# Optimization experiments

Measured on AMD Instinct MI355X. Metric: run time of the kernel, lower is better.

Reference implementation:

```python
import jax, jax.numpy as jnp
import numpy as np

N_TOKENS = 2048
D_MODEL = 1024
D_FF = 4 * D_MODEL
N_EXPERTS = 8
TOP_K = 2


def setup_inputs() -> dict:
    key = jax.random.key(0)
    k_x, k_g, k_w1, k_w2 = jax.random.split(key, 4)
    x = jax.random.normal(k_x, (N_TOKENS, D_MODEL), dtype=jnp.float32)
    # torch Linear stores weight as [out_features, in_features]
    gate_w = jax.random.normal(k_g, (N_EXPERTS, D_MODEL), dtype=jnp.float32) * 0.02
    w1 = jax.random.normal(k_w1, (N_EXPERTS, D_FF, D_MODEL), dtype=jnp.float32) * 0.02
    w2 = jax.random.normal(k_w2, (N_EXPERTS, D_MODEL, D_FF), dtype=jnp.float32) * 0.02
    return {"x": x, "gate_w": gate_w, "w1": w1, "w2": w2}


def reference(x, gate_w, w1, w2):
    # Gating: top-2 logits, softmax over just the selected two logits
    logits = jnp.einsum("nd,ed->ne", x, gate_w)            # [N, E]
    top_vals, top_idx = jax.lax.top_k(logits, TOP_K)         # [N, 2]
    top_w = jax.nn.softmax(top_vals, axis=-1)                # [N, 2]

    # Combine weight per (token, expert): sum of gate weights where routed
    cw = jnp.sum(jax.nn.one_hot(top_idx, N_EXPERTS, dtype=x.dtype)
                 * top_w[..., None], axis=1)                 # [N, E]

    # Per-expert FFN, masked-combined (single-process path of the module)
    out = jnp.zeros_like(x)
    for e in range(N_EXPERTS):
        h = jax.nn.gelu(x @ w1[e].T, approximate=False)      # [N, 4d] (nn.GELU = exact erf)
        y = h @ w2[e].T                                      # [N, d]
        out = out + cw[:, e:e + 1] * y
    return out
```

## Files before the change

kernel.cpp:

```cpp
#include <hip/hip_runtime.h>
#include <hip/hip_bf16.h>

typedef short short8 __attribute__((ext_vector_type(8)));
typedef float f32x4 __attribute__((ext_vector_type(4)));

#define N_TOKENS 2048
#define D_MODEL 1024
#define D_FF 4096
#define N_EXPERTS 8
#define TOTAL_SLOTS (N_TOKENS * 2)
#define BK 32
#define SPLITK2 4
#define KC2 (D_FF / SPLITK2)

static __device__ __forceinline__ unsigned int f2u(float f) {
    union { float f; unsigned int u; } v; v.f = f; return v.u;
}

static __device__ __forceinline__ unsigned short f2bf(float f) {
    unsigned int u = f2u(f);
    unsigned int r = (u + 0x7fffu + ((u >> 16) & 1u)) >> 16;
    return (unsigned short)r;
}

static __device__ __forceinline__ unsigned int pk2bf(float a, float b) {
    __hip_bfloat162 t = __float22bfloat162_rn(float2{a, b});
    unsigned int u;
    __builtin_memcpy(&u, &t, 4);
    return u;
}

typedef __attribute__((address_space(1))) const unsigned int GU;
typedef __attribute__((address_space(3))) unsigned int LU;
static __device__ __forceinline__ void gload_lds16(const void* g, void* l) {
    __builtin_amdgcn_global_load_lds((GU*)g, (LU*)l, 16, 0, 0);
}

__global__ __launch_bounds__(256) void cvt_x_kernel(const float* __restrict__ x,
                                                    unsigned short* __restrict__ xb) {
    int i = (blockIdx.x * 256 + threadIdx.x) * 4;
    if (i >= N_TOKENS * D_MODEL) return;
    float4 f = *(const float4*)(x + i);
    uint2 o;
    o.x = pk2bf(f.x, f.y);
    o.y = pk2bf(f.z, f.w);
    *(uint2*)(xb + i) = o;
}

__global__ __launch_bounds__(64) void gate_kernel(const float* __restrict__ x,
                                                  const float* __restrict__ gw,
                                                  int* __restrict__ counts,
                                                  int* __restrict__ tok_e,
                                                  float* __restrict__ tok_w) {
    const int n = blockIdx.x;
    const int lane = threadIdx.x;
    float p[N_EXPERTS];
#pragma unroll
    for (int e = 0; e < N_EXPERTS; ++e) p[e] = 0.f;
    const float* xr = x + n * D_MODEL;
    for (int d = lane; d < D_MODEL; d += 64) {
        float xv = xr[d];
#pragma unroll
        for (int e = 0; e < N_EXPERTS; ++e) p[e] += xv * gw[e * D_MODEL + d];
    }
#pragma unroll
    for (int e = 0; e < N_EXPERTS; ++e) {
        float v = p[e];
        for (int o = 32; o > 0; o >>= 1) v += __shfl_down(v, o);
        p[e] = v;
    }
    if (lane == 0) {
        int b1 = 0; float v1 = p[0];
        for (int e = 1; e < N_EXPERTS; ++e) if (p[e] > v1) { v1 = p[e]; b1 = e; }
        int b2 = -1; float v2 = -1e30f;
        for (int e = 0; e < N_EXPERTS; ++e) if (e != b1 && p[e] > v2) { v2 = p[e]; b2 = e; }
        float e2 = __expf(v2 - v1);
        float s = 1.f + e2;
        tok_e[n * 2 + 0] = b1; tok_w[n * 2 + 0] = 1.f / s;
        tok_e[n * 2 + 1] = b2; tok_w[n * 2 + 1] = e2 / s;
        atomicAdd(&counts[b1], 1);
        atomicAdd(&counts[b2], 1);
    }
}

__global__ void scan_kernel(const int* __restrict__ counts,
                            int* __restrict__ offsets, int* __restrict__ fill) {
    if (threadIdx.x == 0 && blockIdx.x == 0) {
        int s = 0;
        for (int e = 0; e < N_EXPERTS; ++e) { offsets[e] = s; fill[e] = s; s += counts[e]; }
    }
}

__global__ __launch_bounds__(256) void route_kernel(const int* __restrict__ tok_e,
                                                    const float* __restrict__ tok_w,
                                                    int* __restrict__ fill,
                                                    int* __restrict__ rows_tok,
                                                    float* __restrict__ rows_w) {
    int i = blockIdx.x * 256 + threadIdx.x;
    if (i >= TOTAL_SLOTS) return;
    int e = tok_e[i];
    float w = tok_w[i];
    int pos = atomicAdd(&fill[e], 1);
    rows_tok[pos] = i >> 1;
    rows_w[pos] = w;
}

__global__ __launch_bounds__(256, 3) void gemm1_kernel(const unsigned short* __restrict__ xb,
                                                       const float* __restrict__ w1,
                                                       const int* __restrict__ counts,
                                                       const int* __restrict__ offsets,
                                                       const int* __restrict__ rows_tok,
                                                       unsigned short* __restrict__ h) {
    const int e = blockIdx.z;
    const int cnt = counts[e];
    const int mt = blockIdx.y;
    if (mt * 128 >= cnt) return;
    const int off = offsets[e];
    const int nt = blockIdx.x;

    __shared__ unsigned short As[2][128 * 32];
    __shared__ unsigned short Bs[2][128 * 32];

    const int tid = threadIdx.x;
    const int lane = tid & 63;
    const int wave = tid >> 6;
    const int wm = wave >> 1, wn = wave & 1;

    const int arow = wave * 32 + (lane >> 2);
    const int ac8 = lane & 3;
    int r0 = off + mt * 128 + arow;
    int r1 = r0 + 16;
    r0 = min(r0, TOTAL_SLOTS - 1);
    r1 = min(r1, TOTAL_SLOTS - 1);
    const unsigned short* ag0 = xb + (size_t)rows_tok[r0] * D_MODEL + ac8 * 8;
    const unsigned short* ag1 = xb + (size_t)rows_tok[r1] * D_MODEL + ac8 * 8;
    unsigned short* al0_0 = &As[0][(wave * 32) * 32];
    unsigned short* al1_0 = &As[0][(wave * 32 + 16) * 32];
    unsigned short* al0_1 = &As[1][(wave * 32) * 32];
    unsigned short* al1_1 = &As[1][(wave * 32 + 16) * 32];

    const int brow = tid >> 1, bcol = (tid & 1) * 16;
    const float* bg = w1 + (size_t)e * (D_FF * D_MODEL) + (size_t)(nt * 128 + brow) * D_MODEL + bcol;

    f32x4 acc[4][4];
#pragma unroll
    for (int i = 0; i < 4; ++i)
#pragma unroll
        for (int j = 0; j < 4; ++j) acc[i][j] = (f32x4){0.f, 0.f, 0.f, 0.f};

    {
        gload_lds16(ag0, al0_0);
        gload_lds16(ag1, al1_0);
        float4 fb0 = *(const float4*)(bg + 0);
        float4 fb1 = *(const float4*)(bg + 4);
        float4 fb2 = *(const float4*)(bg + 8);
        float4 fb3 = *(const float4*)(bg + 12);
        unsigned int bp[8];
        bp[0] = pk2bf(fb0.x, fb0.y); bp[1] = pk2bf(fb0.z, fb0.w);
        bp[2] = pk2bf(fb1.x, fb1.y); bp[3] = pk2bf(fb1.z, fb1.w);
        bp[4] = pk2bf(fb2.x, fb2.y); bp[5] = pk2bf(fb2.z, fb2.w);
        bp[6] = pk2bf(fb3.x, fb3.y); bp[7] = pk2bf(fb3.z, fb3.w);
        *(uint4*)&Bs[0][brow * 32 + bcol]     = *(uint4*)&bp[0];
        *(uint4*)&Bs[0][brow * 32 + bcol + 8] = *(uint4*)&bp[4];
    }
    __syncthreads();

    const int KSTEPS = D_MODEL / BK;
#pragma unroll 2
    for (int t = 0; t < KSTEPS; ++t) {
        const int cur = t & 1;
        const bool more = (t + 1 < KSTEPS);
        float4 fb0, fb1, fb2, fb3;
        if (more) {
            const int k1 = (t + 1) * BK;
            fb0 = *(const float4*)(bg + k1 + 0);
            fb1 = *(const float4*)(bg + k1 + 4);
            fb2 = *(const float4*)(bg + k1 + 8);
            fb3 = *(const float4*)(bg + k1 + 12);
            gload_lds16(ag0 + k1, cur ? al0_0 : al0_1);
            gload_lds16(ag1 + k1, cur ? al1_0 : al1_1);
        }
        short8 af[4], bfr[4];
#pragma unroll
        for (int mi = 0; mi < 4; ++mi)
            af[mi] = *(const short8*)&As[cur][(wm * 64 + mi * 16 + (lane & 15)) * 32 + (lane >> 4) * 8];
#pragma unroll
        for (int nj = 0; nj < 4; ++nj)
            bfr[nj] = *(const short8*)&Bs[cur][(wn * 64 + nj * 16 + (lane & 15)) * 32 + (lane >> 4) * 8];
#pragma unroll
        for (int mi = 0; mi < 4; ++mi)
#pragma unroll
            for (int nj = 0; nj < 4; ++nj)
                acc[mi][nj] = __builtin_amdgcn_mfma_f32_16x16x32_bf16(af[mi], bfr[nj], acc[mi][nj], 0, 0, 0);
        if (more) {
            unsigned int bp[8];
            bp[0] = pk2bf(fb0.x, fb0.y); bp[1] = pk2bf(fb0.z, fb0.w);
            bp[2] = pk2bf(fb1.x, fb1.y); bp[3] = pk2bf(fb1.z, fb1.w);
            bp[4] = pk2bf(fb2.x, fb2.y); bp[5] = pk2bf(fb2.z, fb2.w);
            bp[6] = pk2bf(fb3.x, fb3.y); bp[7] = pk2bf(fb3.z, fb3.w);
            const int nb = cur ^ 1;
            *(uint4*)&Bs[nb][brow * 32 + bcol]     = *(uint4*)&bp[0];
            *(uint4*)&Bs[nb][brow * 32 + bcol + 8] = *(uint4*)&bp[4];
        }
        __syncthreads();
    }

    const int lr = (lane >> 4) * 4, lc = lane & 15;
#pragma unroll
    for (int mi = 0; mi < 4; ++mi) {
        const int mbase = mt * 128 + wm * 64 + mi * 16 + lr;
#pragma unroll
        for (int j = 0; j < 4; ++j) {
            const int m = mbase + j;
            if (m < cnt) {
#pragma unroll
                for (int nj = 0; nj < 4; ++nj) {
                    const int n = nt * 128 + wn * 64 + nj * 16 + lc;
                    float v = acc[mi][nj][j];
                    v = 0.5f * v * (1.0f + erff(v * 0.70710678118654752f));
                    h[(size_t)(off + m) * D_FF + n] = f2bf(v);
                }
            }
        }
    }
}

__global__ __launch_bounds__(256, 3) void gemm2_kernel(const unsigned short* __restrict__ h,
                                                       const float* __restrict__ w2,
                                                       const int* __restrict__ counts,
                                                       const int* __restrict__ offsets,
                                                       const int* __restrict__ rows_tok,
                                                       const float* __restrict__ rows_w,
                                                       float* __restrict__ out) {
    const int e = blockIdx.z >> 2;
    const int kc = blockIdx.z & 3;
    const int cnt = counts[e];
    const int mt = blockIdx.y;
    if (mt * 128 >= cnt) return;
    const int off = offsets[e];
    const int nt = blockIdx.x;

    __shared__ unsigned short As[2][128 * 32];
    __shared__ unsigned short Bs[2][128 * 32];

    const int tid = threadIdx.x;
    const int lane = tid & 63;
    const int wave = tid >> 6;
    const int wm = wave >> 1, wn = wave & 1;

    const int arow = wave * 32 + (lane >> 2);
    const int ac8 = lane & 3;
    int r0 = off + mt * 128 + arow;
    int r1 = r0 + 16;
    r0 = min(r0, TOTAL_SLOTS - 1);
    r1 = min(r1, TOTAL_SLOTS - 1);
    const unsigned short* ag0 = h + (size_t)r0 * D_FF + kc * KC2 + ac8 * 8;
    const unsigned short* ag1 = h + (size_t)r1 * D_FF + kc * KC2 + ac8 * 8;
    unsigned short* al0_0 = &As[0][(wave * 32) * 32];
    unsigned short* al1_0 = &As[0][(wave * 32 + 16) * 32];
    unsigned short* al0_1 = &As[1][(wave * 32) * 32];
    unsigned short* al1_1 = &As[1][(wave * 32 + 16) * 32];

    const int brow = tid >> 1, bcol = (tid & 1) * 16;
    const float* bg = w2 + (size_t)e * (D_MODEL * D_FF) + (size_t)(nt * 128 + brow) * D_FF
                      + kc * KC2 + bcol;

    f32x4 acc[4][4];
#pragma unroll
    for (int i = 0; i < 4; ++i)
#pragma unroll
        for (int j = 0; j < 4; ++j) acc[i][j] = (f32x4){0.f, 0.f, 0.f, 0.f};

    {
        gload_lds16(ag0, al0_0);
        gload_lds16(ag1, al1_0);
        float4 fb0 = *(const float4*)(bg + 0);
        float4 fb1 = *(const float4*)(bg + 4);
        float4 fb2 = *(const float4*)(bg + 8);
        float4 fb3 = *(const float4*)(bg + 12);
        unsigned int bp[8];
        bp[0] = pk2bf(fb0.x, fb0.y); bp[1] = pk2bf(fb0.z, fb0.w);
        bp[2] = pk2bf(fb1.x, fb1.y); bp[3] = pk2bf(fb1.z, fb1.w);
        bp[4] = pk2bf(fb2.x, fb2.y); bp[5] = pk2bf(fb2.z, fb2.w);
        bp[6] = pk2bf(fb3.x, fb3.y); bp[7] = pk2bf(fb3.z, fb3.w);
        *(uint4*)&Bs[0][brow * 32 + bcol]     = *(uint4*)&bp[0];
        *(uint4*)&Bs[0][brow * 32 + bcol + 8] = *(uint4*)&bp[4];
    }
    __syncthreads();

    const int KSTEPS = KC2 / BK;
#pragma unroll 2
    for (int t = 0; t < KSTEPS; ++t) {
        const int cur = t & 1;
        const bool more = (t + 1 < KSTEPS);
        float4 fb0, fb1, fb2, fb3;
        if (more) {
            const int k1 = (t + 1) * BK;
            fb0 = *(const float4*)(bg + k1 + 0);
            fb1 = *(const float4*)(bg + k1 + 4);
            fb2 = *(const float4*)(bg + k1 + 8);
            fb3 = *(const float4*)(bg + k1 + 12);
            gload_lds16(ag0 + k1, cur ? al0_0 : al0_1);
            gload_lds16(ag1 + k1, cur ? al1_0 : al1_1);
        }
        short8 af[4], bfr[4];
#pragma unroll
        for (int mi = 0; mi < 4; ++mi)
            af[mi] = *(const short8*)&As[cur][(wm * 64 + mi * 16 + (lane & 15)) * 32 + (lane >> 4) * 8];
#pragma unroll
        for (int nj = 0; nj < 4; ++nj)
            bfr[nj] = *(const short8*)&Bs[cur][(wn * 64 + nj * 16 + (lane & 15)) * 32 + (lane >> 4) * 8];
#pragma unroll
        for (int mi = 0; mi < 4; ++mi)
#pragma unroll
            for (int nj = 0; nj < 4; ++nj)
                acc[mi][nj] = __builtin_amdgcn_mfma_f32_16x16x32_bf16(af[mi], bfr[nj], acc[mi][nj], 0, 0, 0);
        if (more) {
            unsigned int bp[8];
            bp[0] = pk2bf(fb0.x, fb0.y); bp[1] = pk2bf(fb0.z, fb0.w);
            bp[2] = pk2bf(fb1.x, fb1.y); bp[3] = pk2bf(fb1.z, fb1.w);
            bp[4] = pk2bf(fb2.x, fb2.y); bp[5] = pk2bf(fb2.z, fb2.w);
            bp[6] = pk2bf(fb3.x, fb3.y); bp[7] = pk2bf(fb3.z, fb3.w);
            const int nb = cur ^ 1;
            *(uint4*)&Bs[nb][brow * 32 + bcol]     = *(uint4*)&bp[0];
            *(uint4*)&Bs[nb][brow * 32 + bcol + 8] = *(uint4*)&bp[4];
        }
        __syncthreads();
    }

    const int lr = (lane >> 4) * 4, lc = lane & 15;
#pragma unroll
    for (int mi = 0; mi < 4; ++mi) {
        const int mbase = mt * 128 + wm * 64 + mi * 16 + lr;
#pragma unroll
        for (int j = 0; j < 4; ++j) {
            const int m = mbase + j;
            if (m < cnt) {
                const int tok = rows_tok[off + m];
                const float w = rows_w[off + m];
#pragma unroll
                for (int nj = 0; nj < 4; ++nj) {
                    const int n = nt * 128 + wn * 64 + nj * 16 + lc;
                    atomicAdd(&out[(size_t)tok * D_MODEL + n], w * acc[mi][nj][j]);
                }
            }
        }
    }
}


extern "C" void kernel_launch(void* const* d_in, const int* in_sizes, int n_in,
                              void* d_out, int out_size, void* d_ws, size_t ws_size,
                              hipStream_t stream) {
    const float* x  = (const float*)d_in[0];
    const float* gw = (const float*)d_in[1];
    const float* w1 = (const float*)d_in[2];
    const float* w2 = (const float*)d_in[3];
    float* out = (float*)d_out;

    char* ws = (char*)d_ws;
    int*   counts   = (int*)(ws + 0);
    int*   fill     = (int*)(ws + 256);
    int*   offsets  = (int*)(ws + 512);
    int*   tok_e    = (int*)(ws + 768);
    float* tok_w    = (float*)(ws + 17152);
    int*   rows_tok = (int*)(ws + 33536);
    float* rows_w   = (float*)(ws + 49920);
    unsigned short* xb = (unsigned short*)(ws + 66560);
    unsigned short* h  = (unsigned short*)(ws + 66560 + (size_t)N_TOKENS * D_MODEL * 2);

    hipMemsetAsync(counts, 0, 32, stream);
    hipMemsetAsync(d_out, 0, (size_t)out_size * sizeof(float), stream);

    cvt_x_kernel<<<dim3((N_TOKENS * D_MODEL / 4 + 255) / 256), dim3(256), 0, stream>>>(x, xb);
    gate_kernel<<<dim3(N_TOKENS), dim3(64), 0, stream>>>(x, gw, counts, tok_e, tok_w);
    scan_kernel<<<dim3(1), dim3(64), 0, stream>>>(counts, offsets, fill);
    route_kernel<<<dim3((TOTAL_SLOTS + 255) / 256), dim3(256), 0, stream>>>(tok_e, tok_w, fill, rows_tok, rows_w);
    gemm1_kernel<<<dim3(D_FF / 128, 16, N_EXPERTS), dim3(256), 0, stream>>>(xb, w1, counts, offsets, rows_tok, h);
    gemm2_kernel<<<dim3(D_MODEL / 128, 16, N_EXPERTS * SPLITK2), dim3(256), 0, stream>>>(h, w2, counts, offsets, rows_tok, rows_w, out);
}
```

Baseline: 334.8 us.

## Deepen B-operand prefetch to two steps with manual waitcnt and barriers

Both GEMM kernels now prefetch the fp32 weight tile two K-steps ahead into ping-pong register sets, while the A tile is still loaded one step ahead directly into LDS. __syncthreads is replaced by explicit s_waitcnt lgkmcnt/vmcnt counts, s_barrier and sched_barrier so global weight loads stay in flight across the barrier. This targets the weight-load latency that was exposed each iteration. In exchange it raises register pressure and depends on hand-counted vmcnt values being correct.

```diff
diff --git a/kernel.cpp b/kernel.cpp
--- a/kernel.cpp
+++ b/kernel.cpp
@@ -105,6 +105,76 @@
     rows_w[pos] = w;
 }
 
+#define GEMM_BODY(T, CUR, BU, BF, ALn0, ALn1)                                       \
+  {                                                                                 \
+    const int t_ = (T);                                                             \
+    const bool hasA_ = (t_ + 1 < KSTEPS);                                           \
+    const bool hasB_ = (t_ + 2 < KSTEPS);                                           \
+    if (hasA_) {                                                                    \
+      const int k1_ = (t_ + 1) * BK;                                                \
+      gload_lds16(ag0 + k1_, ALn0);                                                 \
+      gload_lds16(ag1 + k1_, ALn1);                                                 \
+    }                                                                               \
+    asm volatile("" ::: "memory");                                                  \
+    if (hasB_) {                                                                    \
+      const int k2_ = (t_ + 2) * BK;                                                \
+      BU##_0 = *(const float4*)(bg + k2_ + 0);                                      \
+      BU##_1 = *(const float4*)(bg + k2_ + 4);                                      \
+      BU##_2 = *(const float4*)(bg + k2_ + 8);                                      \
+      BU##_3 = *(const float4*)(bg + k2_ + 12);                                     \
+    }                                                                               \
+    __builtin_amdgcn_sched_barrier(0);                                              \
+    short8 af_[4], bf_[4];                                                          \
+    _Pragma("unroll") for (int mi = 0; mi < 4; ++mi)                                \
+      af_[mi] = *(const short8*)&As[CUR][(wm * 64 + mi * 16 + (lane & 15)) * 32 + (lane >> 4) * 8]; \
+    _Pragma("unroll") for (int nj = 0; nj < 4; ++nj)                                \
+      bf_[nj] = *(const short8*)&Bs[CUR][(wn * 64 + nj * 16 + (lane & 15)) * 32 + (lane >> 4) * 8]; \
+    _Pragma("unroll") for (int mi = 0; mi < 4; ++mi)                                \
+      _Pragma("unroll") for (int nj = 0; nj < 4; ++nj)                              \
+        acc[mi][nj] = __builtin_amdgcn_mfma_f32_16x16x32_bf16(af_[mi], bf_[nj], acc[mi][nj], 0, 0, 0); \
+    if (hasA_) {                                                                    \
+      unsigned int bp_[8];                                                          \
+      bp_[0] = pk2bf(BF##_0.x, BF##_0.y); bp_[1] = pk2bf(BF##_0.z, BF##_0.w);       \
+      bp_[2] = pk2bf(BF##_1.x, BF##_1.y); bp_[3] = pk2bf(BF##_1.z, BF##_1.w);       \
+      bp_[4] = pk2bf(BF##_2.x, BF##_2.y); bp_[5] = pk2bf(BF##_2.z, BF##_2.w);       \
+      bp_[6] = pk2bf(BF##_3.x, BF##_3.y); bp_[7] = pk2bf(BF##_3.z, BF##_3.w);       \
+      *(uint4*)&Bs[(CUR) ^ 1][brow * 32 + bcol]     = *(uint4*)&bp_[0];             \
+      *(uint4*)&Bs[(CUR) ^ 1][brow * 32 + bcol + 8] = *(uint4*)&bp_[4];             \
+      asm volatile("s_waitcnt lgkmcnt(0)" ::: "memory");                            \
+      if (hasB_) asm volatile("s_waitcnt vmcnt(4)" ::: "memory");                   \
+      else       asm volatile("s_waitcnt vmcnt(0)" ::: "memory");                   \
+      __builtin_amdgcn_s_barrier();                                                 \
+      asm volatile("" ::: "memory");                                                \
+    }                                                                               \
+  }
+
+#define GEMM_PROLOGUE(BE)                                                           \
+  {                                                                                 \
+    gload_lds16(ag0, al0_0);                                                        \
+    gload_lds16(ag1, al1_0);                                                        \
+    asm volatile("" ::: "memory");                                                  \
+    float4 p0 = *(const float4*)(bg + 0);                                           \
+    float4 p1 = *(const float4*)(bg + 4);                                           \
+    float4 p2 = *(const float4*)(bg + 8);                                           \
+    float4 p3 = *(const float4*)(bg + 12);                                          \
+    BE##_0 = *(const float4*)(bg + BK + 0);                                         \
+    BE##_1 = *(const float4*)(bg + BK + 4);                                         \
+    BE##_2 = *(const float4*)(bg + BK + 8);                                         \
+    BE##_3 = *(const float4*)(bg + BK + 12);                                        \
+    __builtin_amdgcn_sched_barrier(0);                                              \
+    unsigned int bp_[8];                                                            \
+    bp_[0] = pk2bf(p0.x, p0.y); bp_[1] = pk2bf(p0.z, p0.w);                         \
+    bp_[2] = pk2bf(p1.x, p1.y); bp_[3] = pk2bf(p1.z, p1.w);                         \
+    bp_[4] = pk2bf(p2.x, p2.y); bp_[5] = pk2bf(p2.z, p2.w);                         \
+    bp_[6] = pk2bf(p3.x, p3.y); bp_[7] = pk2bf(p3.z, p3.w);                         \
+    *(uint4*)&Bs[0][brow * 32 + bcol]     = *(uint4*)&bp_[0];                       \
+    *(uint4*)&Bs[0][brow * 32 + bcol + 8] = *(uint4*)&bp_[4];                       \
+    asm volatile("s_waitcnt lgkmcnt(0)" ::: "memory");                              \
+    asm volatile("s_waitcnt vmcnt(4)" ::: "memory");                                \
+    __builtin_amdgcn_s_barrier();                                                   \
+    asm volatile("" ::: "memory");                                                  \
+  }
+
 __global__ __launch_bounds__(256, 3) void gemm1_kernel(const unsigned short* __restrict__ xb,
                                                        const float* __restrict__ w1,
                                                        const int* __restrict__ counts,
@@ -148,61 +218,14 @@
 #pragma unroll
         for (int j = 0; j < 4; ++j) acc[i][j] = (f32x4){0.f, 0.f, 0.f, 0.f};
 
-    {
-        gload_lds16(ag0, al0_0);
-        gload_lds16(ag1, al1_0);
-        float4 fb0 = *(const float4*)(bg + 0);
-        float4 fb1 = *(const float4*)(bg + 4);
-        float4 fb2 = *(const float4*)(bg + 8);
-        float4 fb3 = *(const float4*)(bg + 12);
-        unsigned int bp[8];
-        bp[0] = pk2bf(fb0.x, fb0.y); bp[1] = pk2bf(fb0.z, fb0.w);
-        bp[2] = pk2bf(fb1.x, fb1.y); bp[3] = pk2bf(fb1.z, fb1.w);
-        bp[4] = pk2bf(fb2.x, fb2.y); bp[5] = pk2bf(fb2.z, fb2.w);
-        bp[6] = pk2bf(fb3.x, fb3.y); bp[7] = pk2bf(fb3.z, fb3.w);
-        *(uint4*)&Bs[0][brow * 32 + bcol]     = *(uint4*)&bp[0];
-        *(uint4*)&Bs[0][brow * 32 + bcol + 8] = *(uint4*)&bp[4];
-    }
-    __syncthreads();
+    float4 bEn_0{0,0,0,0}, bEn_1{0,0,0,0}, bEn_2{0,0,0,0}, bEn_3{0,0,0,0};
+    float4 bOn_0{0,0,0,0}, bOn_1{0,0,0,0}, bOn_2{0,0,0,0}, bOn_3{0,0,0,0};
 
     const int KSTEPS = D_MODEL / BK;
-#pragma unroll 2
-    for (int t = 0; t < KSTEPS; ++t) {
-        const int cur = t & 1;
-        const bool more = (t + 1 < KSTEPS);
-        float4 fb0, fb1, fb2, fb3;
-        if (more) {
-            const int k1 = (t + 1) * BK;
-            fb0 = *(const float4*)(bg + k1 + 0);
-            fb1 = *(const float4*)(bg + k1 + 4);
-            fb2 = *(const float4*)(bg + k1 + 8);
-            fb3 = *(const float4*)(bg + k1 + 12);
-            gload_lds16(ag0 + k1, cur ? al0_0 : al0_1);
-            gload_lds16(ag1 + k1, cur ? al1_0 : al1_1);
-        }
-        short8 af[4], bfr[4];
-#pragma unroll
-        for (int mi = 0; mi < 4; ++mi)
-            af[mi] = *(const short8*)&As[cur][(wm * 64 + mi * 16 + (lane & 15)) * 32 + (lane >> 4) * 8];
-#pragma unroll
-        for (int nj = 0; nj < 4; ++nj)
-            bfr[nj] = *(const short8*)&Bs[cur][(wn * 64 + nj * 16 + (lane & 15)) * 32 + (lane >> 4) * 8];
-#pragma unroll
-        for (int mi = 0; mi < 4; ++mi)
-#pragma unroll
-            for (int nj = 0; nj < 4; ++nj)
-                acc[mi][nj] = __builtin_amdgcn_mfma_f32_16x16x32_bf16(af[mi], bfr[nj], acc[mi][nj], 0, 0, 0);
-        if (more) {
-            unsigned int bp[8];
-            bp[0] = pk2bf(fb0.x, fb0.y); bp[1] = pk2bf(fb0.z, fb0.w);
-            bp[2] = pk2bf(fb1.x, fb1.y); bp[3] = pk2bf(fb1.z, fb1.w);
-            bp[4] = pk2bf(fb2.x, fb2.y); bp[5] = pk2bf(fb2.z, fb2.w);
-            bp[6] = pk2bf(fb3.x, fb3.y); bp[7] = pk2bf(fb3.z, fb3.w);
-            const int nb = cur ^ 1;
-            *(uint4*)&Bs[nb][brow * 32 + bcol]     = *(uint4*)&bp[0];
-            *(uint4*)&Bs[nb][brow * 32 + bcol + 8] = *(uint4*)&bp[4];
-        }
-        __syncthreads();
+    GEMM_PROLOGUE(bEn)
+    for (int tt = 0; tt < KSTEPS; tt += 2) {
+        GEMM_BODY(tt,     0, bOn, bEn, al0_1, al1_1)
+        GEMM_BODY(tt + 1, 1, bEn, bOn, al0_0, al1_0)
     }
 
     const int lr = (lane >> 4) * 4, lc = lane & 15;
@@ -271,61 +294,14 @@
 #pragma unroll
         for (int j = 0; j < 4; ++j) acc[i][j] = (f32x4){0.f, 0.f, 0.f, 0.f};
 
-    {
-        gload_lds16(ag0, al0_0);
-        gload_lds16(ag1, al1_0);
-        float4 fb0 = *(const float4*)(bg + 0);
-        float4 fb1 = *(const float4*)(bg + 4);
-        float4 fb2 = *(const float4*)(bg + 8);
-        float4 fb3 = *(const float4*)(bg + 12);
-        unsigned int bp[8];
-        bp[0] = pk2bf(fb0.x, fb0.y); bp[1] = pk2bf(fb0.z, fb0.w);
-        bp[2] = pk2bf(fb1.x, fb1.y); bp[3] = pk2bf(fb1.z, fb1.w);
-        bp[4] = pk2bf(fb2.x, fb2.y); bp[5] = pk2bf(fb2.z, fb2.w);
-        bp[6] = pk2bf(fb3.x, fb3.y); bp[7] = pk2bf(fb3.z, fb3.w);
-        *(uint4*)&Bs[0][brow * 32 + bcol]     = *(uint4*)&bp[0];
-        *(uint4*)&Bs[0][brow * 32 + bcol + 8] = *(uint4*)&bp[4];
-    }
-    __syncthreads();
+    float4 bEn_0{0,0,0,0}, bEn_1{0,0,0,0}, bEn_2{0,0,0,0}, bEn_3{0,0,0,0};
+    float4 bOn_0{0,0,0,0}, bOn_1{0,0,0,0}, bOn_2{0,0,0,0}, bOn_3{0,0,0,0};
 
     const int KSTEPS = KC2 / BK;
-#pragma unroll 2
-    for (int t = 0; t < KSTEPS; ++t) {
-        const int cur = t & 1;
-        const bool more = (t + 1 < KSTEPS);
-        float4 fb0, fb1, fb2, fb3;
-        if (more) {
-            const int k1 = (t + 1) * BK;
-            fb0 = *(const float4*)(bg + k1 + 0);
-            fb1 = *(const float4*)(bg + k1 + 4);
-            fb2 = *(const float4*)(bg + k1 + 8);
-            fb3 = *(const float4*)(bg + k1 + 12);
-            gload_lds16(ag0 + k1, cur ? al0_0 : al0_1);
-            gload_lds16(ag1 + k1, cur ? al1_0 : al1_1);
-        }
-        short8 af[4], bfr[4];
-#pragma unroll
-        for (int mi = 0; mi < 4; ++mi)
-            af[mi] = *(const short8*)&As[cur][(wm * 64 + mi * 16 + (lane & 15)) * 32 + (lane >> 4) * 8];
-#pragma unroll
-        for (int nj = 0; nj < 4; ++nj)
-            bfr[nj] = *(const short8*)&Bs[cur][(wn * 64 + nj * 16 + (lane & 15)) * 32 + (lane >> 4) * 8];
-#pragma unroll
-        for (int mi = 0; mi < 4; ++mi)
-#pragma unroll
-            for (int nj = 0; nj < 4; ++nj)
-                acc[mi][nj] = __builtin_amdgcn_mfma_f32_16x16x32_bf16(af[mi], bfr[nj], acc[mi][nj], 0, 0, 0);
-        if (more) {
-            unsigned int bp[8];
-            bp[0] = pk2bf(fb0.x, fb0.y); bp[1] = pk2bf(fb0.z, fb0.w);
-            bp[2] = pk2bf(fb1.x, fb1.y); bp[3] = pk2bf(fb1.z, fb1.w);
-            bp[4] = pk2bf(fb2.x, fb2.y); bp[5] = pk2bf(fb2.z, fb2.w);
-            bp[6] = pk2bf(fb3.x, fb3.y); bp[7] = pk2bf(fb3.z, fb3.w);
-            const int nb = cur ^ 1;
-            *(uint4*)&Bs[nb][brow * 32 + bcol]     = *(uint4*)&bp[0];
-            *(uint4*)&Bs[nb][brow * 32 + bcol + 8] = *(uint4*)&bp[4];
-        }
-        __syncthreads();
+    GEMM_PROLOGUE(bEn)
+    for (int tt = 0; tt < KSTEPS; tt += 2) {
+        GEMM_BODY(tt,     0, bOn, bEn, al0_1, al1_1)
+        GEMM_BODY(tt + 1, 1, bEn, bOn, al0_0, al1_0)
     }
 
     const int lr = (lane >> 4) * 4, lc = lane & 15;
```

Measured after the change: 325.0 us. 1.03x faster.

## Pre-convert expert weights to bf16 and stream them into LDS directly

Applied to the files above, without the earlier changes.

Adds a grid-stride kernel that converts w1 and w2 from fp32 to bf16 into the workspace on every call. The GEMM kernels are templated so that, when the workspace is large enough, B tiles are loaded with global_load_lds exactly like A tiles. This removes the in-loop fp32 loads, the bf16 packing and the register-staged LDS writes. It costs an extra full pass over the weights (read fp32, write bf16) before the GEMMs, and it raises the launch-bounds occupancy hint from 3 to 4.

```diff
diff --git a/kernel.cpp b/kernel.cpp
--- a/kernel.cpp
+++ b/kernel.cpp
@@ -34,6 +34,22 @@
 typedef __attribute__((address_space(3))) unsigned int LU;
 static __device__ __forceinline__ void gload_lds16(const void* g, void* l) {
     __builtin_amdgcn_global_load_lds((GU*)g, (LU*)l, 16, 0, 0);
+}
+
+__global__ __launch_bounds__(256) void cvt_w_kernel(const float* __restrict__ src,
+                                                    unsigned short* __restrict__ dst,
+                                                    int n8) {
+    int i = blockIdx.x * 256 + threadIdx.x;
+    const int stride = gridDim.x * 256;
+    for (; i < n8; i += stride) {
+        const size_t b = (size_t)i * 8;
+        float4 f0 = *(const float4*)(src + b);
+        float4 f1 = *(const float4*)(src + b + 4);
+        uint4 o;
+        o.x = pk2bf(f0.x, f0.y); o.y = pk2bf(f0.z, f0.w);
+        o.z = pk2bf(f1.x, f1.y); o.w = pk2bf(f1.z, f1.w);
+        *(uint4*)(dst + b) = o;
+    }
 }
 
 __global__ __launch_bounds__(256) void cvt_x_kernel(const float* __restrict__ x,
@@ -105,12 +121,14 @@
     rows_w[pos] = w;
 }
 
-__global__ __launch_bounds__(256, 3) void gemm1_kernel(const unsigned short* __restrict__ xb,
-                                                       const float* __restrict__ w1,
-                                                       const int* __restrict__ counts,
-                                                       const int* __restrict__ offsets,
-                                                       const int* __restrict__ rows_tok,
-                                                       unsigned short* __restrict__ h) {
+template <bool PRE>
+__global__ __launch_bounds__(256, 4) void gemm1_kernel(
+    const unsigned short* __restrict__ xb,
+    const unsigned short* __restrict__ w1b,
+    const float* __restrict__ w1f,
+    const int* __restrict__ counts, const int* __restrict__ offsets,
+    const int* __restrict__ rows_tok,
+    unsigned short* __restrict__ h) {
     const int e = blockIdx.z;
     const int cnt = counts[e];
     const int mt = blockIdx.y;
@@ -121,26 +139,21 @@
     __shared__ unsigned short As[2][128 * 32];
     __shared__ unsigned short Bs[2][128 * 32];
 
-    const int tid = threadIdx.x;
-    const int lane = tid & 63;
-    const int wave = tid >> 6;
+    const int tid = threadIdx.x, lane = tid & 63, wave = tid >> 6;
     const int wm = wave >> 1, wn = wave & 1;
 
-    const int arow = wave * 32 + (lane >> 2);
     const int ac8 = lane & 3;
-    int r0 = off + mt * 128 + arow;
+    int r0 = off + mt * 128 + wave * 32 + (lane >> 2);
     int r1 = r0 + 16;
     r0 = min(r0, TOTAL_SLOTS - 1);
     r1 = min(r1, TOTAL_SLOTS - 1);
     const unsigned short* ag0 = xb + (size_t)rows_tok[r0] * D_MODEL + ac8 * 8;
     const unsigned short* ag1 = xb + (size_t)rows_tok[r1] * D_MODEL + ac8 * 8;
-    unsigned short* al0_0 = &As[0][(wave * 32) * 32];
-    unsigned short* al1_0 = &As[0][(wave * 32 + 16) * 32];
-    unsigned short* al0_1 = &As[1][(wave * 32) * 32];
-    unsigned short* al1_1 = &As[1][(wave * 32 + 16) * 32];
-
+
+    const int bgrow = nt * 128 + wave * 32 + (lane >> 2);
+    const unsigned short* bg0 = w1b + (size_t)e * (D_FF * D_MODEL) + (size_t)bgrow * D_MODEL + ac8 * 8;
     const int brow = tid >> 1, bcol = (tid & 1) * 16;
-    const float* bg = w1 + (size_t)e * (D_FF * D_MODEL) + (size_t)(nt * 128 + brow) * D_MODEL + bcol;
+    const float* bgf = w1f + (size_t)e * (D_FF * D_MODEL) + (size_t)(nt * 128 + brow) * D_MODEL + bcol;
 
     f32x4 acc[4][4];
 #pragma unroll
@@ -148,37 +161,56 @@
 #pragma unroll
         for (int j = 0; j < 4; ++j) acc[i][j] = (f32x4){0.f, 0.f, 0.f, 0.f};
 
-    {
-        gload_lds16(ag0, al0_0);
-        gload_lds16(ag1, al1_0);
-        float4 fb0 = *(const float4*)(bg + 0);
-        float4 fb1 = *(const float4*)(bg + 4);
-        float4 fb2 = *(const float4*)(bg + 8);
-        float4 fb3 = *(const float4*)(bg + 12);
+    auto stageA = [&](int buf, int t) {
+        const int k = t * BK;
+        gload_lds16(ag0 + k, &As[buf][(wave * 32) * 32]);
+        gload_lds16(ag1 + k, &As[buf][(wave * 32 + 16) * 32]);
+    };
+    auto stageBpre = [&](int buf, int t) {
+        const int k = t * BK;
+        gload_lds16(bg0 + k, &Bs[buf][(wave * 32) * 32]);
+        gload_lds16(bg0 + 16 * D_MODEL + k, &Bs[buf][(wave * 32 + 16) * 32]);
+    };
+    auto writeBf32 = [&](int buf, const float4& f0, const float4& f1,
+                         const float4& f2, const float4& f3) {
         unsigned int bp[8];
-        bp[0] = pk2bf(fb0.x, fb0.y); bp[1] = pk2bf(fb0.z, fb0.w);
-        bp[2] = pk2bf(fb1.x, fb1.y); bp[3] = pk2bf(fb1.z, fb1.w);
-        bp[4] = pk2bf(fb2.x, fb2.y); bp[5] = pk2bf(fb2.z, fb2.w);
-        bp[6] = pk2bf(fb3.x, fb3.y); bp[7] = pk2bf(fb3.z, fb3.w);
-        *(uint4*)&Bs[0][brow * 32 + bcol]     = *(uint4*)&bp[0];
-        *(uint4*)&Bs[0][brow * 32 + bcol + 8] = *(uint4*)&bp[4];
+        bp[0] = pk2bf(f0.x, f0.y); bp[1] = pk2bf(f0.z, f0.w);
+        bp[2] = pk2bf(f1.x, f1.y); bp[3] = pk2bf(f1.z, f1.w);
+        bp[4] = pk2bf(f2.x, f2.y); bp[5] = pk2bf(f2.z, f2.w);
+        bp[6] = pk2bf(f3.x, f3.y); bp[7] = pk2bf(f3.z, f3.w);
+        *(uint4*)&Bs[buf][brow * 32 + bcol]     = *(uint4*)&bp[0];
+        *(uint4*)&Bs[buf][brow * 32 + bcol + 8] = *(uint4*)&bp[4];
+    };
+
+    stageA(0, 0);
+    if constexpr (PRE) {
+        stageBpre(0, 0);
+    } else {
+        float4 f0 = *(const float4*)(bgf + 0);
+        float4 f1 = *(const float4*)(bgf + 4);
+        float4 f2 = *(const float4*)(bgf + 8);
+        float4 f3 = *(const float4*)(bgf + 12);
+        writeBf32(0, f0, f1, f2, f3);
     }
     __syncthreads();
 
     const int KSTEPS = D_MODEL / BK;
 #pragma unroll 2
     for (int t = 0; t < KSTEPS; ++t) {
-        const int cur = t & 1;
+        const int cur = t & 1, nxt = cur ^ 1;
         const bool more = (t + 1 < KSTEPS);
-        float4 fb0, fb1, fb2, fb3;
+        float4 f0, f1, f2, f3;
         if (more) {
-            const int k1 = (t + 1) * BK;
-            fb0 = *(const float4*)(bg + k1 + 0);
-            fb1 = *(const float4*)(bg + k1 + 4);
-            fb2 = *(const float4*)(bg + k1 + 8);
-            fb3 = *(const float4*)(bg + k1 + 12);
-            gload_lds16(ag0 + k1, cur ? al0_0 : al0_1);
-            gload_lds16(ag1 + k1, cur ? al1_0 : al1_1);
+            stageA(nxt, t + 1);
+            if constexpr (PRE) {
+                stageBpre(nxt, t + 1);
+            } else {
+                const int k = (t + 1) * BK;
+                f0 = *(const float4*)(bgf + k + 0);
+                f1 = *(const float4*)(bgf + k + 4);
+                f2 = *(const float4*)(bgf + k + 8);
+                f3 = *(const float4*)(bgf + k + 12);
+            }
         }
         short8 af[4], bfr[4];
 #pragma unroll
@@ -192,15 +224,8 @@
 #pragma unroll
             for (int nj = 0; nj < 4; ++nj)
                 acc[mi][nj] = __builtin_amdgcn_mfma_f32_16x16x32_bf16(af[mi], bfr[nj], acc[mi][nj], 0, 0, 0);
-        if (more) {
-            unsigned int bp[8];
-            bp[0] = pk2bf(fb0.x, fb0.y); bp[1] = pk2bf(fb0.z, fb0.w);
-            bp[2] = pk2bf(fb1.x, fb1.y); bp[3] = pk2bf(fb1.z, fb1.w);
-            bp[4] = pk2bf(fb2.x, fb2.y); bp[5] = pk2bf(fb2.z, fb2.w);
-            bp[6] = pk2bf(fb3.x, fb3.y); bp[7] = pk2bf(fb3.z, fb3.w);
-            const int nb = cur ^ 1;
-            *(uint4*)&Bs[nb][brow * 32 + bcol]     = *(uint4*)&bp[0];
-            *(uint4*)&Bs[nb][brow * 32 + bcol + 8] = *(uint4*)&bp[4];
+        if constexpr (!PRE) {
+            if (more) writeBf32(nxt, f0, f1, f2, f3);
         }
         __syncthreads();
     }
@@ -225,13 +250,14 @@
     }
 }
 
-__global__ __launch_bounds__(256, 3) void gemm2_kernel(const unsigned short* __restrict__ h,
-                                                       const float* __restrict__ w2,
-                                                       const int* __restrict__ counts,
-                                                       const int* __restrict__ offsets,
-                                                       const int* __restrict__ rows_tok,
-                                                       const float* __restrict__ rows_w,
-                                                       float* __restrict__ out) {
+template <bool PRE>
+__global__ __launch_bounds__(256, 4) void gemm2_kernel(
+    const unsigned short* __restrict__ h,
+    const unsigned short* __restrict__ w2b,
+    const float* __restrict__ w2f,
+    const int* __restrict__ counts, const int* __restrict__ offsets,
+    const int* __restrict__ rows_tok, const float* __restrict__ rows_w,
+    float* __restrict__ out) {
     const int e = blockIdx.z >> 2;
     const int kc = blockIdx.z & 3;
     const int cnt = counts[e];
@@ -243,27 +269,21 @@
     __shared__ unsigned short As[2][128 * 32];
     __shared__ unsigned short Bs[2][128 * 32];
 
-    const int tid = threadIdx.x;
-    const int lane = tid & 63;
-    const int wave = tid >> 6;
+    const int tid = threadIdx.x, lane = tid & 63, wave = tid >> 6;
     const int wm = wave >> 1, wn = wave & 1;
 
-    const int arow = wave * 32 + (lane >> 2);
     const int ac8 = lane & 3;
-    int r0 = off + mt * 128 + arow;
+    int r0 = off + mt * 128 + wave * 32 + (lane >> 2);
     int r1 = r0 + 16;
     r0 = min(r0, TOTAL_SLOTS - 1);
     r1 = min(r1, TOTAL_SLOTS - 1);
     const unsigned short* ag0 = h + (size_t)r0 * D_FF + kc * KC2 + ac8 * 8;
     const unsigned short* ag1 = h + (size_t)r1 * D_FF + kc * KC2 + ac8 * 8;
-    unsigned short* al0_0 = &As[0][(wave * 32) * 32];
-    unsigned short* al1_0 = &As[0][(wave * 32 + 16) * 32];
-    unsigned short* al0_1 = &As[1][(wave * 32) * 32];
-    unsigned short* al1_1 = &As[1][(wave * 32 + 16) * 32];
-
+
+    const int bgrow = nt * 128 + wave * 32 + (lane >> 2);
+    const unsigned short* bg0 = w2b + (size_t)e * (D_MODEL * D_FF) + (size_t)bgrow * D_FF + kc * KC2 + ac8 * 8;
     const int brow = tid >> 1, bcol = (tid & 1) * 16;
-    const float* bg = w2 + (size_t)e * (D_MODEL * D_FF) + (size_t)(nt * 128 + brow) * D_FF
-                      + kc * KC2 + bcol;
+    const float* bgf = w2f + (size_t)e * (D_MODEL * D_FF) + (size_t)(nt * 128 + brow) * D_FF + kc * KC2 + bcol;
 
     f32x4 acc[4][4];
 #pragma unroll
@@ -271,37 +291,56 @@
 #pragma unroll
         for (int j = 0; j < 4; ++j) acc[i][j] = (f32x4){0.f, 0.f, 0.f, 0.f};
 
-    {
-        gload_lds16(ag0, al0_0);
-        gload_lds16(ag1, al1_0);
-        float4 fb0 = *(const float4*)(bg + 0);
-        float4 fb1 = *(const float4*)(bg + 4);
-        float4 fb2 = *(const float4*)(bg + 8);
-        float4 fb3 = *(const float4*)(bg + 12);
+    auto stageA = [&](int buf, int t) {
+        const int k = t * BK;
+        gload_lds16(ag0 + k, &As[buf][(wave * 32) * 32]);
+        gload_lds16(ag1 + k, &As[buf][(wave * 32 + 16) * 32]);
+    };
+    auto stageBpre = [&](int buf, int t) {
+        const int k = t * BK;
+        gload_lds16(bg0 + k, &Bs[buf][(wave * 32) * 32]);
+        gload_lds16(bg0 + 16 * D_FF + k, &Bs[buf][(wave * 32 + 16) * 32]);
+    };
+    auto writeBf32 = [&](int buf, const float4& f0, const float4& f1,
+                         const float4& f2, const float4& f3) {
         unsigned int bp[8];
-        bp[0] = pk2bf(fb0.x, fb0.y); bp[1] = pk2bf(fb0.z, fb0.w);
-        bp[2] = pk2bf(fb1.x, fb1.y); bp[3] = pk2bf(fb1.z, fb1.w);
-        bp[4] = pk2bf(fb2.x, fb2.y); bp[5] = pk2bf(fb2.z, fb2.w);
-        bp[6] = pk2bf(fb3.x, fb3.y); bp[7] = pk2bf(fb3.z, fb3.w);
-        *(uint4*)&Bs[0][brow * 32 + bcol]     = *(uint4*)&bp[0];
-        *(uint4*)&Bs[0][brow * 32 + bcol + 8] = *(uint4*)&bp[4];
+        bp[0] = pk2bf(f0.x, f0.y); bp[1] = pk2bf(f0.z, f0.w);
+        bp[2] = pk2bf(f1.x, f1.y); bp[3] = pk2bf(f1.z, f1.w);
+        bp[4] = pk2bf(f2.x, f2.y); bp[5] = pk2bf(f2.z, f2.w);
+        bp[6] = pk2bf(f3.x, f3.y); bp[7] = pk2bf(f3.z, f3.w);
+        *(uint4*)&Bs[buf][brow * 32 + bcol]     = *(uint4*)&bp[0];
+        *(uint4*)&Bs[buf][brow * 32 + bcol + 8] = *(uint4*)&bp[4];
+    };
+
+    stageA(0, 0);
+    if constexpr (PRE) {
+        stageBpre(0, 0);
+    } else {
+        float4 f0 = *(const float4*)(bgf + 0);
+        float4 f1 = *(const float4*)(bgf + 4);
+        float4 f2 = *(const float4*)(bgf + 8);
+        float4 f3 = *(const float4*)(bgf + 12);
+        writeBf32(0, f0, f1, f2, f3);
     }
     __syncthreads();
 
     const int KSTEPS = KC2 / BK;
 #pragma unroll 2
     for (int t = 0; t < KSTEPS; ++t) {
-        const int cur = t & 1;
+        const int cur = t & 1, nxt = cur ^ 1;
         const bool more = (t + 1 < KSTEPS);
-        float4 fb0, fb1, fb2, fb3;
+        float4 f0, f1, f2, f3;
         if (more) {
-            const int k1 = (t + 1) * BK;
-            fb0 = *(const float4*)(bg + k1 + 0);
-            fb1 = *(const float4*)(bg + k1 + 4);
-            fb2 = *(const float4*)(bg + k1 + 8);
-            fb3 = *(const float4*)(bg + k1 + 12);
-            gload_lds16(ag0 + k1, cur ? al0_0 : al0_1);
-            gload_lds16(ag1 + k1, cur ? al1_0 : al1_1);
+            stageA(nxt, t + 1);
+            if constexpr (PRE) {
+                stageBpre(nxt, t + 1);
+            } else {
+                const int k = (t + 1) * BK;
+                f0 = *(const float4*)(bgf + k + 0);
+                f1 = *(const float4*)(bgf + k + 4);
+                f2 = *(const float4*)(bgf + k + 8);
+                f3 = *(const float4*)(bgf + k + 12);
+            }
         }
         short8 af[4], bfr[4];
 #pragma unroll
@@ -315,15 +354,8 @@
 #pragma unroll
             for (int nj = 0; nj < 4; ++nj)
                 acc[mi][nj] = __builtin_amdgcn_mfma_f32_16x16x32_bf16(af[mi], bfr[nj], acc[mi][nj], 0, 0, 0);
-        if (more) {
-            unsigned int bp[8];
-            bp[0] = pk2bf(fb0.x, fb0.y); bp[1] = pk2bf(fb0.z, fb0.w);
-            bp[2] = pk2bf(fb1.x, fb1.y); bp[3] = pk2bf(fb1.z, fb1.w);
-            bp[4] = pk2bf(fb2.x, fb2.y); bp[5] = pk2bf(fb2.z, fb2.w);
-            bp[6] = pk2bf(fb3.x, fb3.y); bp[7] = pk2bf(fb3.z, fb3.w);
-            const int nb = cur ^ 1;
-            *(uint4*)&Bs[nb][brow * 32 + bcol]     = *(uint4*)&bp[0];
-            *(uint4*)&Bs[nb][brow * 32 + bcol + 8] = *(uint4*)&bp[4];
+        if constexpr (!PRE) {
+            if (more) writeBf32(nxt, f0, f1, f2, f3);
         }
         __syncthreads();
     }
@@ -366,16 +398,34 @@
     float* tok_w    = (float*)(ws + 17152);
     int*   rows_tok = (int*)(ws + 33536);
     float* rows_w   = (float*)(ws + 49920);
-    unsigned short* xb = (unsigned short*)(ws + 66560);
-    unsigned short* h  = (unsigned short*)(ws + 66560 + (size_t)N_TOKENS * D_MODEL * 2);
+    unsigned short* xb  = (unsigned short*)(ws + 66560);
+    unsigned short* h   = (unsigned short*)(ws + 4260864);
+    unsigned short* w1b = (unsigned short*)(ws + 37815296ull);
+    unsigned short* w2b = (unsigned short*)(ws + 104924160ull);
+    const bool pre = (ws_size >= 172033024ull);
 
     hipMemsetAsync(counts, 0, 32, stream);
     hipMemsetAsync(d_out, 0, (size_t)out_size * sizeof(float), stream);
 
+    if (pre) {
+        const int n8 = (N_EXPERTS * D_FF * D_MODEL) / 8;
+        cvt_w_kernel<<<dim3(2048), dim3(256), 0, stream>>>(w1, w1b, n8);
+        cvt_w_kernel<<<dim3(2048), dim3(256), 0, stream>>>(w2, w2b, n8);
+    }
     cvt_x_kernel<<<dim3((N_TOKENS * D_MODEL / 4 + 255) / 256), dim3(256), 0, stream>>>(x, xb);
     gate_kernel<<<dim3(N_TOKENS), dim3(64), 0, stream>>>(x, gw, counts, tok_e, tok_w);
     scan_kernel<<<dim3(1), dim3(64), 0, stream>>>(counts, offsets, fill);
     route_kernel<<<dim3((TOTAL_SLOTS + 255) / 256), dim3(256), 0, stream>>>(tok_e, tok_w, fill, rows_tok, rows_w);
-    gemm1_kernel<<<dim3(D_FF / 128, 16, N_EXPERTS), dim3(256), 0, stream>>>(xb, w1, counts, offsets, rows_tok, h);
-    gemm2_kernel<<<dim3(D_MODEL / 128, 16, N_EXPERTS * SPLITK2), dim3(256), 0, stream>>>(h, w2, counts, offsets, rows_tok, rows_w, out);
-}
+
+    if (pre) {
+        gemm1_kernel<true><<<dim3(D_FF / 128, 16, N_EXPERTS), dim3(256), 0, stream>>>(
+            xb, w1b, w1, counts, offsets, rows_tok, h);
+        gemm2_kernel<true><<<dim3(D_MODEL / 128, 16, N_EXPERTS * SPLITK2), dim3(256), 0, stream>>>(
+            h, w2b, w2, counts, offsets, rows_tok, rows_w, out);
+    } else {
+        gemm1_kernel<false><<<dim3(D_FF / 128, 16, N_EXPERTS), dim3(256), 0, stream>>>(
+            xb, w1b, w1, counts, offsets, rows_tok, h);
+        gemm2_kernel<false><<<dim3(D_MODEL / 128, 16, N_EXPERTS * SPLITK2), dim3(256), 0, stream>>>(
+            h, w2b, w2, counts, offsets, rows_tok, rows_w, out);
+    }
+}
```

Result: slower. 345.5 us (+3.2%).
